# Optimization experiments

Measured on AMD Instinct MI355X. Metric: run time of the kernel, lower is better.

## Reference

```python
import jax, jax.numpy as jnp
import numpy as np

B, F, V, E, A = 8192, 39, 1_000_000, 16, 16  # batch, fields, vocab, embed, attn


def setup_inputs() -> dict:
    key = jax.random.key(0)
    ks = jax.random.split(key, 9)
    return {
        "feat_index": jax.random.randint(ks[0], (B, F), 0, V),
        "feat_value": jax.random.uniform(ks[1], (B, F), dtype=jnp.float32),
        "first_order_weights": jax.random.normal(ks[2], (V, 1), dtype=jnp.float32) * 0.01,
        "emb_table": jax.random.normal(ks[3], (V, E), dtype=jnp.float32) * 0.01,
        "bias": jax.random.normal(ks[4], (1,), dtype=jnp.float32),
        "attention_w": jax.random.normal(ks[5], (E, A), dtype=jnp.float32) * 0.1,
        "attention_b": jax.random.normal(ks[6], (A,), dtype=jnp.float32) * 0.1,
        "projection_h": jax.random.normal(ks[7], (A, 1), dtype=jnp.float32) * 0.1,
        "projection_p": jax.random.normal(ks[8], (E, 1), dtype=jnp.float32) * 0.1,
    }


def reference(feat_index, feat_value, first_order_weights, emb_table, bias,
              attention_w, attention_b, projection_h, projection_p):
    fv = feat_value[..., None]                                  # [B,F,1]
    # first order: gather weights, scale by value, sum over fields
    y_first = jnp.sum(first_order_weights[feat_index] * fv, axis=1)[:, 0]  # [B]
    # embeddings scaled by feature values
    emb = emb_table[feat_index] * fv                            # [B,F,E]
    # pairwise bi-interaction over all i<j field pairs (num_pairs = F*(F-1)/2)
    iu, ju = np.triu_indices(F, k=1)
    bi = emb[:, iu, :] * emb[:, ju, :]                          # [B,P,E]
    # tiny attention MLP + softmax over pairs
    att = jax.nn.relu(jnp.einsum('bpe,ea->bpa', bi, attention_w) + attention_b)
    score = jax.nn.softmax(jnp.einsum('bpa,ao->bpo', att, projection_h), axis=1)  # [B,P,1]
    pooled = jnp.sum(score * bi, axis=1)                        # [B,E]
    aw = (pooled @ projection_p)[:, 0]                          # [B]
    y = bias + y_first + aw                                     # [B]
    return jax.nn.sigmoid(y)
```

## Files before the change

### kernel.cpp

```cpp
#include <hip/hip_runtime.h>
#include <hip/hip_fp16.h>
#include <math.h>


#define BB 8192
#define FF 39
#define PP 741
#define NT 24
#define RBYTES 48
#define SBYTES (FF * RBYTES)

typedef _Float16 f16x8 __attribute__((ext_vector_type(8)));
typedef _Float16 h2    __attribute__((ext_vector_type(2)));
typedef __fp16   hw2   __attribute__((ext_vector_type(2)));
typedef float    f32x4  __attribute__((ext_vector_type(4)));
typedef float    f32x16 __attribute__((ext_vector_type(16)));

struct alignas(16) PijT { unsigned v[32][NT]; };
static constexpr PijT make_pij() {
    PijT t{};
    int p = 0;
    for (int i = 0; i < FF; ++i)
        for (int j = i + 1; j < FF; ++j) {
            t.v[p & 31][p >> 5] =
                ((unsigned)(i * RBYTES) << 16) | (unsigned)(j * RBYTES);
            ++p;
        }
    return t;
}
__device__ constexpr PijT c_pij = make_pij();

static __device__ __forceinline__ h2 cvt2(float lo, float hi) {
    return __builtin_bit_cast(h2, __builtin_amdgcn_cvt_pkrtz(lo, hi));
}
static __device__ __forceinline__ h2 ash2(unsigned d) {
    return __builtin_bit_cast(h2, d);
}
static __device__ __forceinline__ float fdot2f(h2 a, h2 b, float c) {
    return __builtin_amdgcn_fdot2(__builtin_bit_cast(hw2, a),
                                  __builtin_bit_cast(hw2, b), c, false);
}
static __device__ __forceinline__ h2 relu2(h2 x) {
    const h2 zz = {(_Float16)0.f, (_Float16)0.f};
    return __builtin_elementwise_max(x, zz);
}

__global__ __launch_bounds__(256, 5)
void afm_kernel(const int*   __restrict__ fidx,
                const float* __restrict__ fval,
                const float* __restrict__ fow,
                const float* __restrict__ emb,
                const float* __restrict__ bias,
                const float* __restrict__ aw_,
                const float* __restrict__ ab_,
                const float* __restrict__ ph_,
                const float* __restrict__ pp_,
                float*       __restrict__ out)
{
    __shared__ __align__(16) unsigned char s_emb[4 * SBYTES];

    const int tid  = threadIdx.x;
    const int wid  = tid >> 6;
    const int lane = tid & 63;
    const int n    = lane & 31;
    const int h    = lane >> 5;
    const int smp  = blockIdx.x * 4 + wid;

    int ixr = 0; float vr = 0.f;
    if (lane < FF) {
        ixr = fidx[smp * FF + lane];
        vr  = fval[smp * FF + lane];
    }

    unsigned char* my = s_emb + wid * SBYTES;
    for (int u = lane; u < FF * 2; u += 64) {
        int row = u >> 1, hh = u & 1;
        int   ix = __shfl(ixr, row);
        float v  = __shfl(vr,  row);
        const float4* src = (const float4*)emb + (size_t)ix * 4 + hh * 2;
        float4 e0 = src[0], e1 = src[1];
        h2 a0 = cvt2(e0.x * v, e0.y * v);
        h2 a1 = cvt2(e0.z * v, e0.w * v);
        h2 a2 = cvt2(e1.x * v, e1.y * v);
        h2 a3 = cvt2(e1.z * v, e1.w * v);
        uint4 d = make_uint4(__builtin_bit_cast(unsigned, a0),
                             __builtin_bit_cast(unsigned, a1),
                             __builtin_bit_cast(unsigned, a2),
                             __builtin_bit_cast(unsigned, a3));
        *(uint4*)(my + row * RBYTES + hh * 16) = d;
    }

    float fo = (lane < FF) ? fow[ixr] * vr : 0.f;

    const float LOG2E = 1.44269504088896f;
    h2 hp0, hp1, hp2, hp3;
    {
        const f32x4 lo = ((const f32x4*)ph_)[h];
        const f32x4 hi = ((const f32x4*)ph_)[h + 2];
        hp0 = cvt2(lo[0] * LOG2E, lo[1] * LOG2E);
        hp1 = cvt2(lo[2] * LOG2E, lo[3] * LOG2E);
        hp2 = cvt2(hi[0] * LOG2E, hi[1] * LOG2E);
        hp3 = cvt2(hi[2] * LOG2E, hi[3] * LOG2E);
    }

    f32x16 cinit;
    {
        const f32x4 ab_lo = ((const f32x4*)ab_)[h];
        const f32x4 ab_hi = ((const f32x4*)ab_)[h + 2];
        cinit[0] = ab_lo[0]; cinit[1] = ab_lo[1];
        cinit[2] = ab_lo[2]; cinit[3] = ab_lo[3];
        cinit[4] = ab_hi[0]; cinit[5] = ab_hi[1];
        cinit[6] = ab_hi[2]; cinit[7] = ab_hi[3];
        #pragma unroll
        for (int r = 8; r < 16; ++r) cinit[r] = 0.f;
    }

    f16x8 wfrag;
    {
        float t0 = 0.f, t1 = 0.f, t2 = 0.f, t3 = 0.f,
              t4 = 0.f, t5 = 0.f, t6 = 0.f, t7 = 0.f;
        if (n < 16) {
            const float* base = aw_ + (8 * h) * 16 + n;
            t0 = base[0];   t1 = base[16];  t2 = base[32];  t3 = base[48];
            t4 = base[64];  t5 = base[80];  t6 = base[96];  t7 = base[112];
        } else if (n == 16) {
            const float* base = pp_ + 8 * h;
            t0 = base[0]; t1 = base[1]; t2 = base[2]; t3 = base[3];
            t4 = base[4]; t5 = base[5]; t6 = base[6]; t7 = base[7];
        }
        union { h2 hh[4]; f16x8 v; } u;
        u.hh[0] = cvt2(t0, t1); u.hh[1] = cvt2(t2, t3);
        u.hh[2] = cvt2(t4, t5); u.hh[3] = cvt2(t6, t7);
        wfrag = u.v;
    }

    unsigned po[NT];
    {
        const uint4* myp4 = (const uint4*)c_pij.v[n];
        #pragma unroll
        for (int g = 0; g < 6; ++g) {
            uint4 q = myp4[g];
            po[4 * g + 0] = q.x; po[4 * g + 1] = q.y;
            po[4 * g + 2] = q.z; po[4 * g + 3] = q.w;
        }
    }

    const unsigned char* bpre = my + h * 16;
    float aw = 0.f;
    float z  = 0.f;

    uint4 di = *(const uint4*)(bpre + (po[0] >> 16));
    uint4 dj = *(const uint4*)(bpre + (po[0] & 0xFFFFu));

    #pragma unroll
    for (int t = 0; t < NT; ++t) {
        uint4 diN = di, djN = dj;
        if (t + 1 < NT) {
            diN = *(const uint4*)(bpre + (po[t + 1] >> 16));
            djN = *(const uint4*)(bpre + (po[t + 1] & 0xFFFFu));
        }
        h2 m0 = ash2(di.x) * ash2(dj.x);
        h2 m1 = ash2(di.y) * ash2(dj.y);
        h2 m2 = ash2(di.z) * ash2(dj.z);
        h2 m3 = ash2(di.w) * ash2(dj.w);
        union { h2 hh[4]; f16x8 v; } u;
        u.hh[0] = m0; u.hh[1] = m1; u.hh[2] = m2; u.hh[3] = m3;
        f32x16 d = __builtin_amdgcn_mfma_f32_32x32x16_f16(wfrag, u.v,
                                                          cinit, 0, 0, 0);
        h2 c0 = relu2(cvt2(d[0], d[1]));
        h2 c1 = relu2(cvt2(d[2], d[3]));
        h2 c2 = relu2(cvt2(d[4], d[5]));
        h2 c3 = relu2(cvt2(d[6], d[7]));
        float s = fdot2f(c0, hp0,
                  fdot2f(c1, hp1,
                  fdot2f(c2, hp2,
                  fdot2f(c3, hp3, 0.f))));
        s += __shfl_xor(s, 32);
        float w = __builtin_amdgcn_exp2f(s);
        if (t == NT - 1) w = (n < PP - (NT - 1) * 32) ? w : 0.f;
        z  += w;
        aw  = fmaf(w, d[8], aw);
        di = diN; dj = djN;
    }

    #pragma unroll
    for (int m = 1; m < 64; m <<= 1) {
        aw += __shfl_xor(aw, m);
        z  += __shfl_xor(z, m);
        fo += __shfl_xor(fo, m);
    }
    if (lane == 0) {
        float y = bias[0] + fo + 2.f * aw / z;
        out[smp] = 1.f / (1.f + __expf(-y));
    }
}

extern "C" void kernel_launch(void* const* d_in, const int* in_sizes, int n_in,
                              void* d_out, int out_size, void* d_ws, size_t ws_size,
                              hipStream_t stream) {
    const int*   fidx      = (const int*)  d_in[0];
    const float* fval      = (const float*)d_in[1];
    const float* fow       = (const float*)d_in[2];
    const float* emb_table = (const float*)d_in[3];
    const float* bias      = (const float*)d_in[4];
    const float* attn_w    = (const float*)d_in[5];
    const float* attn_b    = (const float*)d_in[6];
    const float* proj_h    = (const float*)d_in[7];
    const float* proj_p    = (const float*)d_in[8];
    float* out = (float*)d_out;

    afm_kernel<<<BB / 4, 256, 0, stream>>>(fidx, fval, fow, emb_table, bias,
                                           attn_w, attn_b, proj_h, proj_p, out);
}
```

Baseline: 124.6 us.

## Prefetch next sample's embeddings via async global-to-LDS loads, two samples per wave

Each wave now handles two samples. Embedding rows are gathered straight into an LDS staging buffer with global_load_lds, and the second sample's gather is issued while the first sample's pairwise and attention compute runs. The intent is to hide the latency of the random gather behind compute. The cost is more LDS per wave (staging plus the fp16 buffer), launch bounds lowered from 5 to 4 blocks, half as many blocks, and explicit waitcnt barriers.

```diff
diff --git a/kernel.cpp b/kernel.cpp
--- a/kernel.cpp
+++ b/kernel.cpp
@@ -9,6 +9,10 @@
 #define NT 24
 #define RBYTES 48
 #define SBYTES (FF * RBYTES)
+#define STGB   (FF * 64)
+#define CH     (FF * 4)
+#define SPW    2
+#define WLDS   (STGB + SBYTES)
 
 typedef _Float16 f16x8 __attribute__((ext_vector_type(8)));
 typedef _Float16 h2    __attribute__((ext_vector_type(2)));
@@ -45,7 +49,13 @@
     return __builtin_elementwise_max(x, zz);
 }
 
-__global__ __launch_bounds__(256, 5)
+static __device__ __forceinline__ void gld_lds16(const void* g, void* l) {
+    __builtin_amdgcn_global_load_lds(
+        (const __attribute__((address_space(1))) void*)g,
+        (__attribute__((address_space(3))) void*)l, 16, 0, 0);
+}
+
+__global__ __launch_bounds__(256, 4)
 void afm_kernel(const int*   __restrict__ fidx,
                 const float* __restrict__ fval,
                 const float* __restrict__ fow,
@@ -57,141 +67,174 @@
                 const float* __restrict__ pp_,
                 float*       __restrict__ out)
 {
-    __shared__ __align__(16) unsigned char s_emb[4 * SBYTES];
+    __shared__ __align__(16) unsigned char s_all[4 * WLDS];
 
     const int tid  = threadIdx.x;
     const int wid  = tid >> 6;
     const int lane = tid & 63;
     const int n    = lane & 31;
     const int h    = lane >> 5;
-    const int smp  = blockIdx.x * 4 + wid;
-
-    int ixr = 0; float vr = 0.f;
+    const int s0   = (blockIdx.x * 4 + wid) * SPW;
+
+    unsigned char* stg = s_all + wid * WLDS;
+    unsigned char* my  = stg + STGB;
+
+    int idxA = 0, idxB = 0; float vA = 0.f, vB = 0.f;
     if (lane < FF) {
-        ixr = fidx[smp * FF + lane];
-        vr  = fval[smp * FF + lane];
-    }
-
-    unsigned char* my = s_emb + wid * SBYTES;
-    for (int u = lane; u < FF * 2; u += 64) {
-        int row = u >> 1, hh = u & 1;
-        int   ix = __shfl(ixr, row);
-        float v  = __shfl(vr,  row);
-        const float4* src = (const float4*)emb + (size_t)ix * 4 + hh * 2;
-        float4 e0 = src[0], e1 = src[1];
-        h2 a0 = cvt2(e0.x * v, e0.y * v);
-        h2 a1 = cvt2(e0.z * v, e0.w * v);
-        h2 a2 = cvt2(e1.x * v, e1.y * v);
-        h2 a3 = cvt2(e1.z * v, e1.w * v);
-        uint4 d = make_uint4(__builtin_bit_cast(unsigned, a0),
-                             __builtin_bit_cast(unsigned, a1),
-                             __builtin_bit_cast(unsigned, a2),
-                             __builtin_bit_cast(unsigned, a3));
-        *(uint4*)(my + row * RBYTES + hh * 16) = d;
-    }
-
-    float fo = (lane < FF) ? fow[ixr] * vr : 0.f;
+        idxA = fidx[s0 * FF + lane];
+        vA   = fval[s0 * FF + lane];
+        idxB = fidx[(s0 + 1) * FF + lane];
+        vB   = fval[(s0 + 1) * FF + lane];
+    }
 
     const float LOG2E = 1.44269504088896f;
-    h2 hp0, hp1, hp2, hp3;
+    const f32x4 ph_lo = ((const f32x4*)ph_)[h];
+    const f32x4 ph_hi = ((const f32x4*)ph_)[h + 2];
+    const f32x4 ab_lo = ((const f32x4*)ab_)[h];
+    const f32x4 ab_hi = ((const f32x4*)ab_)[h + 2];
+    float t0 = 0.f, t1 = 0.f, t2 = 0.f, t3 = 0.f,
+          t4 = 0.f, t5 = 0.f, t6 = 0.f, t7 = 0.f;
+    if (n < 16) {
+        const float* base = aw_ + (8 * h) * 16 + n;
+        t0 = base[0];   t1 = base[16];  t2 = base[32];  t3 = base[48];
+        t4 = base[64];  t5 = base[80];  t6 = base[96];  t7 = base[112];
+    } else if (n == 16) {
+        const float* base = pp_ + 8 * h;
+        t0 = base[0]; t1 = base[1]; t2 = base[2]; t3 = base[3];
+        t4 = base[4]; t5 = base[5]; t6 = base[6]; t7 = base[7];
+    }
+    unsigned po[NT];
     {
-        const f32x4 lo = ((const f32x4*)ph_)[h];
-        const f32x4 hi = ((const f32x4*)ph_)[h + 2];
-        hp0 = cvt2(lo[0] * LOG2E, lo[1] * LOG2E);
-        hp1 = cvt2(lo[2] * LOG2E, lo[3] * LOG2E);
-        hp2 = cvt2(hi[0] * LOG2E, hi[1] * LOG2E);
-        hp3 = cvt2(hi[2] * LOG2E, hi[3] * LOG2E);
-    }
+        const uint4* myp4 = (const uint4*)c_pij.v[n];
+        #pragma unroll
+        for (int g = 0; g < 6; ++g) {
+            uint4 q = myp4[g];
+            po[4 * g + 0] = q.x; po[4 * g + 1] = q.y;
+            po[4 * g + 2] = q.z; po[4 * g + 3] = q.w;
+        }
+    }
+
+    float foA = (lane < FF) ? fow[idxA] : 0.f;
+    float foB = (lane < FF) ? fow[idxB] : 0.f;
+
+    const int r0 = lane >> 2, r1 = (64 + lane) >> 2, r2 = (128 + lane) >> 2;
+    const int cA0 = __shfl(idxA, r0), cA1 = __shfl(idxA, r1),
+              cA2 = __shfl(idxA, r2);
+    const int cB0 = __shfl(idxB, r0), cB1 = __shfl(idxB, r1),
+              cB2 = __shfl(idxB, r2);
+    const int q4 = (lane & 3) * 4;
+
+    gld_lds16(emb + (size_t)(unsigned)cA0 * 16 + q4, stg);
+    gld_lds16(emb + (size_t)(unsigned)cA1 * 16 + q4, stg + 1024);
+    if (lane < CH - 128)
+        gld_lds16(emb + (size_t)(unsigned)cA2 * 16 + q4, stg + 2048);
+
+    h2 hp0 = cvt2(ph_lo[0] * LOG2E, ph_lo[1] * LOG2E);
+    h2 hp1 = cvt2(ph_lo[2] * LOG2E, ph_lo[3] * LOG2E);
+    h2 hp2 = cvt2(ph_hi[0] * LOG2E, ph_hi[1] * LOG2E);
+    h2 hp3 = cvt2(ph_hi[2] * LOG2E, ph_hi[3] * LOG2E);
 
     f32x16 cinit;
-    {
-        const f32x4 ab_lo = ((const f32x4*)ab_)[h];
-        const f32x4 ab_hi = ((const f32x4*)ab_)[h + 2];
-        cinit[0] = ab_lo[0]; cinit[1] = ab_lo[1];
-        cinit[2] = ab_lo[2]; cinit[3] = ab_lo[3];
-        cinit[4] = ab_hi[0]; cinit[5] = ab_hi[1];
-        cinit[6] = ab_hi[2]; cinit[7] = ab_hi[3];
-        #pragma unroll
-        for (int r = 8; r < 16; ++r) cinit[r] = 0.f;
-    }
+    cinit[0] = ab_lo[0]; cinit[1] = ab_lo[1];
+    cinit[2] = ab_lo[2]; cinit[3] = ab_lo[3];
+    cinit[4] = ab_hi[0]; cinit[5] = ab_hi[1];
+    cinit[6] = ab_hi[2]; cinit[7] = ab_hi[3];
+    #pragma unroll
+    for (int r = 8; r < 16; ++r) cinit[r] = 0.f;
 
     f16x8 wfrag;
     {
-        float t0 = 0.f, t1 = 0.f, t2 = 0.f, t3 = 0.f,
-              t4 = 0.f, t5 = 0.f, t6 = 0.f, t7 = 0.f;
-        if (n < 16) {
-            const float* base = aw_ + (8 * h) * 16 + n;
-            t0 = base[0];   t1 = base[16];  t2 = base[32];  t3 = base[48];
-            t4 = base[64];  t5 = base[80];  t6 = base[96];  t7 = base[112];
-        } else if (n == 16) {
-            const float* base = pp_ + 8 * h;
-            t0 = base[0]; t1 = base[1]; t2 = base[2]; t3 = base[3];
-            t4 = base[4]; t5 = base[5]; t6 = base[6]; t7 = base[7];
-        }
         union { h2 hh[4]; f16x8 v; } u;
         u.hh[0] = cvt2(t0, t1); u.hh[1] = cvt2(t2, t3);
         u.hh[2] = cvt2(t4, t5); u.hh[3] = cvt2(t6, t7);
         wfrag = u.v;
     }
 
-    unsigned po[NT];
-    {
-        const uint4* myp4 = (const uint4*)c_pij.v[n];
-        #pragma unroll
-        for (int g = 0; g < 6; ++g) {
-            uint4 q = myp4[g];
-            po[4 * g + 0] = q.x; po[4 * g + 1] = q.y;
-            po[4 * g + 2] = q.z; po[4 * g + 3] = q.w;
-        }
-    }
-
     const unsigned char* bpre = my + h * 16;
-    float aw = 0.f;
-    float z  = 0.f;
-
-    uint4 di = *(const uint4*)(bpre + (po[0] >> 16));
-    uint4 dj = *(const uint4*)(bpre + (po[0] & 0xFFFFu));
-
-    #pragma unroll
-    for (int t = 0; t < NT; ++t) {
-        uint4 diN = di, djN = dj;
-        if (t + 1 < NT) {
-            diN = *(const uint4*)(bpre + (po[t + 1] >> 16));
-            djN = *(const uint4*)(bpre + (po[t + 1] & 0xFFFFu));
-        }
-        h2 m0 = ash2(di.x) * ash2(dj.x);
-        h2 m1 = ash2(di.y) * ash2(dj.y);
-        h2 m2 = ash2(di.z) * ash2(dj.z);
-        h2 m3 = ash2(di.w) * ash2(dj.w);
-        union { h2 hh[4]; f16x8 v; } u;
-        u.hh[0] = m0; u.hh[1] = m1; u.hh[2] = m2; u.hh[3] = m3;
-        f32x16 d = __builtin_amdgcn_mfma_f32_32x32x16_f16(wfrag, u.v,
-                                                          cinit, 0, 0, 0);
-        h2 c0 = relu2(cvt2(d[0], d[1]));
-        h2 c1 = relu2(cvt2(d[2], d[3]));
-        h2 c2 = relu2(cvt2(d[4], d[5]));
-        h2 c3 = relu2(cvt2(d[6], d[7]));
-        float s = fdot2f(c0, hp0,
-                  fdot2f(c1, hp1,
-                  fdot2f(c2, hp2,
-                  fdot2f(c3, hp3, 0.f))));
-        s += __shfl_xor(s, 32);
-        float w = __builtin_amdgcn_exp2f(s);
-        if (t == NT - 1) w = (n < PP - (NT - 1) * 32) ? w : 0.f;
-        z  += w;
-        aw  = fmaf(w, d[8], aw);
-        di = diN; dj = djN;
-    }
-
-    #pragma unroll
-    for (int m = 1; m < 64; m <<= 1) {
-        aw += __shfl_xor(aw, m);
-        z  += __shfl_xor(z, m);
-        fo += __shfl_xor(fo, m);
-    }
-    if (lane == 0) {
-        float y = bias[0] + fo + 2.f * aw / z;
-        out[smp] = 1.f / (1.f + __expf(-y));
+
+    float vcur = vA, vnxt = vB;
+    float fcur = foA, fnxt = foB;
+
+    #pragma unroll 1
+    for (int s = 0; s < SPW; ++s) {
+        asm volatile("s_waitcnt vmcnt(0)" ::: "memory");
+        __builtin_amdgcn_sched_barrier(0);
+
+        #pragma unroll
+        for (int k = 0; k < 3; ++k) {
+            const int u   = 64 * k + lane;
+            const int row = u >> 2, q = u & 3;
+            const float v = __shfl(vcur, row);
+            if (u < CH) {
+                const f32x4 e = *(const f32x4*)(stg + u * 16);
+                h2 a0 = cvt2(e[0] * v, e[1] * v);
+                h2 a1 = cvt2(e[2] * v, e[3] * v);
+                uint2 dd = make_uint2(__builtin_bit_cast(unsigned, a0),
+                                      __builtin_bit_cast(unsigned, a1));
+                *(uint2*)(my + row * RBYTES + q * 8) = dd;
+            }
+        }
+
+        asm volatile("s_waitcnt lgkmcnt(0)" ::: "memory");
+        __builtin_amdgcn_sched_barrier(0);
+
+        if (s == 0) {
+            gld_lds16(emb + (size_t)(unsigned)cB0 * 16 + q4, stg);
+            gld_lds16(emb + (size_t)(unsigned)cB1 * 16 + q4, stg + 1024);
+            if (lane < CH - 128)
+                gld_lds16(emb + (size_t)(unsigned)cB2 * 16 + q4, stg + 2048);
+        }
+
+        float aw = 0.f;
+        float z  = 0.f;
+
+        uint4 di = *(const uint4*)(bpre + (po[0] >> 16));
+        uint4 dj = *(const uint4*)(bpre + (po[0] & 0xFFFFu));
+
+        #pragma unroll
+        for (int t = 0; t < NT; ++t) {
+            uint4 diN = di, djN = dj;
+            if (t + 1 < NT) {
+                diN = *(const uint4*)(bpre + (po[t + 1] >> 16));
+                djN = *(const uint4*)(bpre + (po[t + 1] & 0xFFFFu));
+            }
+            h2 m0 = ash2(di.x) * ash2(dj.x);
+            h2 m1 = ash2(di.y) * ash2(dj.y);
+            h2 m2 = ash2(di.z) * ash2(dj.z);
+            h2 m3 = ash2(di.w) * ash2(dj.w);
+            union { h2 hh[4]; f16x8 v; } u;
+            u.hh[0] = m0; u.hh[1] = m1; u.hh[2] = m2; u.hh[3] = m3;
+            f32x16 d = __builtin_amdgcn_mfma_f32_32x32x16_f16(wfrag, u.v,
+                                                              cinit, 0, 0, 0);
+            h2 c0 = relu2(cvt2(d[0], d[1]));
+            h2 c1 = relu2(cvt2(d[2], d[3]));
+            h2 c2 = relu2(cvt2(d[4], d[5]));
+            h2 c3 = relu2(cvt2(d[6], d[7]));
+            float sc = fdot2f(c0, hp0,
+                       fdot2f(c1, hp1,
+                       fdot2f(c2, hp2,
+                       fdot2f(c3, hp3, 0.f))));
+            sc += __shfl_xor(sc, 32);
+            float w = __builtin_amdgcn_exp2f(sc);
+            if (t == NT - 1) w = (n < PP - (NT - 1) * 32) ? w : 0.f;
+            z  += w;
+            aw  = fmaf(w, d[8], aw);
+            di = diN; dj = djN;
+        }
+
+        float fo = fcur * vcur;
+        #pragma unroll
+        for (int m = 1; m < 64; m <<= 1) {
+            aw += __shfl_xor(aw, m);
+            z  += __shfl_xor(z, m);
+            fo += __shfl_xor(fo, m);
+        }
+        if (lane == 0) {
+            float y = bias[0] + fo + 2.f * aw / z;
+            out[s0 + s] = 1.f / (1.f + __expf(-y));
+        }
+
+        vcur = vnxt; fcur = fnxt;
     }
 }
 
@@ -209,6 +252,7 @@
     const float* proj_p    = (const float*)d_in[8];
     float* out = (float*)d_out;
 
-    afm_kernel<<<BB / 4, 256, 0, stream>>>(fidx, fval, fow, emb_table, bias,
-                                           attn_w, attn_b, proj_h, proj_p, out);
-}
+    afm_kernel<<<BB / (4 * SPW), 256, 0, stream>>>(fidx, fval, fow, emb_table,
+                                                   bias, attn_w, attn_b,
+                                                   proj_h, proj_p, out);
+}
```

New measurement: 126.9 us. About the same (+1.8%).

## Split embedding gather into separate high-occupancy kernel writing fp16 rows to workspace

Applied to the files above, without the earlier changes.

Moves the random embedding gather, value scaling and fp16 conversion into a separate kernel. That kernel uses one thread per 16-byte chunk and higher occupancy, and writes packed rows plus first-order terms to workspace. The compute kernel then does contiguous coalesced loads from workspace into LDS. The aim is more memory-level parallelism on the latency-bound random gather, at the cost of an extra launch and a workspace round trip. It falls back to the fused kernel when the workspace is too small.

```diff
diff --git a/kernel.cpp b/kernel.cpp
--- a/kernel.cpp
+++ b/kernel.cpp
@@ -9,6 +9,10 @@
 #define NT 24
 #define RBYTES 48
 #define SBYTES (FF * RBYTES)
+#define SF     (BB * FF)
+#define HROWS_B 0
+#define FOWV_B  ((size_t)SF * 32)
+#define WS_NEEDED ((size_t)SF * 36)
 
 typedef _Float16 f16x8 __attribute__((ext_vector_type(8)));
 typedef _Float16 h2    __attribute__((ext_vector_type(2)));
@@ -45,53 +49,11 @@
     return __builtin_elementwise_max(x, zz);
 }
 
-__global__ __launch_bounds__(256, 5)
-void afm_kernel(const int*   __restrict__ fidx,
-                const float* __restrict__ fval,
-                const float* __restrict__ fow,
-                const float* __restrict__ emb,
-                const float* __restrict__ bias,
-                const float* __restrict__ aw_,
-                const float* __restrict__ ab_,
-                const float* __restrict__ ph_,
-                const float* __restrict__ pp_,
-                float*       __restrict__ out)
-{
-    __shared__ __align__(16) unsigned char s_emb[4 * SBYTES];
-
-    const int tid  = threadIdx.x;
-    const int wid  = tid >> 6;
-    const int lane = tid & 63;
-    const int n    = lane & 31;
-    const int h    = lane >> 5;
-    const int smp  = blockIdx.x * 4 + wid;
-
-    int ixr = 0; float vr = 0.f;
-    if (lane < FF) {
-        ixr = fidx[smp * FF + lane];
-        vr  = fval[smp * FF + lane];
-    }
-
-    unsigned char* my = s_emb + wid * SBYTES;
-    for (int u = lane; u < FF * 2; u += 64) {
-        int row = u >> 1, hh = u & 1;
-        int   ix = __shfl(ixr, row);
-        float v  = __shfl(vr,  row);
-        const float4* src = (const float4*)emb + (size_t)ix * 4 + hh * 2;
-        float4 e0 = src[0], e1 = src[1];
-        h2 a0 = cvt2(e0.x * v, e0.y * v);
-        h2 a1 = cvt2(e0.z * v, e0.w * v);
-        h2 a2 = cvt2(e1.x * v, e1.y * v);
-        h2 a3 = cvt2(e1.z * v, e1.w * v);
-        uint4 d = make_uint4(__builtin_bit_cast(unsigned, a0),
-                             __builtin_bit_cast(unsigned, a1),
-                             __builtin_bit_cast(unsigned, a2),
-                             __builtin_bit_cast(unsigned, a3));
-        *(uint4*)(my + row * RBYTES + hh * 16) = d;
-    }
-
-    float fo = (lane < FF) ? fow[ixr] * vr : 0.f;
-
+static __device__ __forceinline__ void afm_body(
+    const unsigned char* my, int lane, int n, int h, float fo,
+    const float* aw_, const float* ab_, const float* ph_, const float* pp_,
+    const float* bias, float* out, int smp)
+{
     const float LOG2E = 1.44269504088896f;
     h2 hp0, hp1, hp2, hp3;
     {
@@ -195,6 +157,118 @@
     }
 }
 
+__global__ __launch_bounds__(256, 8)
+void gather_scale(const int*   __restrict__ fidx,
+                  const float* __restrict__ fval,
+                  const float* __restrict__ fow,
+                  const float* __restrict__ emb,
+                  unsigned char* __restrict__ ws)
+{
+    const int t  = blockIdx.x * 256 + threadIdx.x;
+    const int q  = t & 3;
+    const int sf = t >> 2;
+
+    const int   ix = fidx[sf];
+    const float v  = fval[sf];
+
+    const float4 e = ((const float4*)emb)[(size_t)(unsigned)ix * 4 + q];
+    h2 a0 = cvt2(e.x * v, e.y * v);
+    h2 a1 = cvt2(e.z * v, e.w * v);
+    uint2 d = make_uint2(__builtin_bit_cast(unsigned, a0),
+                         __builtin_bit_cast(unsigned, a1));
+    *(uint2*)(ws + HROWS_B + (size_t)sf * 32 + q * 8) = d;
+
+    if (q == 0)
+        ((float*)(ws + FOWV_B))[sf] = fow[ix] * v;
+}
+
+__global__ __launch_bounds__(256, 5)
+void afm_compute(const unsigned char* __restrict__ ws,
+                 const float* __restrict__ bias,
+                 const float* __restrict__ aw_,
+                 const float* __restrict__ ab_,
+                 const float* __restrict__ ph_,
+                 const float* __restrict__ pp_,
+                 float*       __restrict__ out)
+{
+    __shared__ __align__(16) unsigned char s_emb[4 * SBYTES];
+
+    const int tid  = threadIdx.x;
+    const int wid  = tid >> 6;
+    const int lane = tid & 63;
+    const int n    = lane & 31;
+    const int h    = lane >> 5;
+    const int smp  = blockIdx.x * 4 + wid;
+
+    unsigned char* my = s_emb + wid * SBYTES;
+    const unsigned char* src = ws + HROWS_B + (size_t)smp * (FF * 32);
+    {
+        uint4 d0 = *(const uint4*)(src + lane * 16);
+        int r0 = lane >> 1, h0 = lane & 1;
+        *(uint4*)(my + r0 * RBYTES + h0 * 16) = d0;
+        if (lane < FF * 2 - 64) {
+            uint4 d1 = *(const uint4*)(src + (64 + lane) * 16);
+            int u1 = 64 + lane, r1 = u1 >> 1, h1 = u1 & 1;
+            *(uint4*)(my + r1 * RBYTES + h1 * 16) = d1;
+        }
+    }
+
+    float fo = (lane < FF)
+             ? ((const float*)(ws + FOWV_B))[smp * FF + lane] : 0.f;
+
+    afm_body(my, lane, n, h, fo, aw_, ab_, ph_, pp_, bias, out, smp);
+}
+
+__global__ __launch_bounds__(256, 5)
+void afm_kernel(const int*   __restrict__ fidx,
+                const float* __restrict__ fval,
+                const float* __restrict__ fow,
+                const float* __restrict__ emb,
+                const float* __restrict__ bias,
+                const float* __restrict__ aw_,
+                const float* __restrict__ ab_,
+                const float* __restrict__ ph_,
+                const float* __restrict__ pp_,
+                float*       __restrict__ out)
+{
+    __shared__ __align__(16) unsigned char s_emb[4 * SBYTES];
+
+    const int tid  = threadIdx.x;
+    const int wid  = tid >> 6;
+    const int lane = tid & 63;
+    const int n    = lane & 31;
+    const int h    = lane >> 5;
+    const int smp  = blockIdx.x * 4 + wid;
+
+    int ixr = 0; float vr = 0.f;
+    if (lane < FF) {
+        ixr = fidx[smp * FF + lane];
+        vr  = fval[smp * FF + lane];
+    }
+
+    unsigned char* my = s_emb + wid * SBYTES;
+    for (int u = lane; u < FF * 2; u += 64) {
+        int row = u >> 1, hh = u & 1;
+        int   ix = __shfl(ixr, row);
+        float v  = __shfl(vr,  row);
+        const float4* src = (const float4*)emb + (size_t)ix * 4 + hh * 2;
+        float4 e0 = src[0], e1 = src[1];
+        h2 a0 = cvt2(e0.x * v, e0.y * v);
+        h2 a1 = cvt2(e0.z * v, e0.w * v);
+        h2 a2 = cvt2(e1.x * v, e1.y * v);
+        h2 a3 = cvt2(e1.z * v, e1.w * v);
+        uint4 d = make_uint4(__builtin_bit_cast(unsigned, a0),
+                             __builtin_bit_cast(unsigned, a1),
+                             __builtin_bit_cast(unsigned, a2),
+                             __builtin_bit_cast(unsigned, a3));
+        *(uint4*)(my + row * RBYTES + hh * 16) = d;
+    }
+
+    float fo = (lane < FF) ? fow[ixr] * vr : 0.f;
+
+    afm_body(my, lane, n, h, fo, aw_, ab_, ph_, pp_, bias, out, smp);
+}
+
 extern "C" void kernel_launch(void* const* d_in, const int* in_sizes, int n_in,
                               void* d_out, int out_size, void* d_ws, size_t ws_size,
                               hipStream_t stream) {
@@ -209,6 +283,15 @@
     const float* proj_p    = (const float*)d_in[8];
     float* out = (float*)d_out;
 
-    afm_kernel<<<BB / 4, 256, 0, stream>>>(fidx, fval, fow, emb_table, bias,
-                                           attn_w, attn_b, proj_h, proj_p, out);
-}
+    if (d_ws != nullptr && ws_size >= WS_NEEDED) {
+        unsigned char* ws = (unsigned char*)d_ws;
+        gather_scale<<<(SF * 4) / 256, 256, 0, stream>>>(fidx, fval, fow,
+                                                         emb_table, ws);
+        afm_compute<<<BB / 4, 256, 0, stream>>>(ws, bias, attn_w, attn_b,
+                                                proj_h, proj_p, out);
+    } else {
+        afm_kernel<<<BB / 4, 256, 0, stream>>>(fidx, fval, fow, emb_table,
+                                               bias, attn_w, attn_b,
+                                               proj_h, proj_p, out);
+    }
+}
```

After: 132.9 us. 6.7% more time.
